# Kernel tuning notes

Measured on AMD Instinct MI355X. Metric: run time of the kernel, lower is better.

Reference implementation:

```python
import jax, jax.numpy as jnp
import numpy as np

D_LATENT = 2048
RANK = 16

def setup_inputs() -> dict:
    key = jax.random.key(0)
    k1, k2, k3 = jax.random.split(key, 3)
    h = jax.random.normal(k1, (4, 4096, D_LATENT), dtype=jnp.float32)
    # LoRA params: original init is randn/50 for A, zeros for B; use randn/50 for
    # both so the output is non-trivial for correctness testing.
    mat_A = jax.random.normal(k2, (D_LATENT, RANK), dtype=jnp.float32) / 50.0
    mat_B = jax.random.normal(k3, (RANK, D_LATENT), dtype=jnp.float32) / 50.0
    return {"h": h, "mat_A": mat_A, "mat_B": mat_B}

def reference(h, mat_A, mat_B):
    # Faithful to torch: F.linear(h, A @ B) == h @ (A @ B).T
    W = mat_A @ mat_B                      # [d_latent, d_latent]
    return jnp.einsum('bsd,ed->bse', h, W)  # h @ W.T
```

## Files before the change

kernel.cpp:

```cpp
#include <hip/hip_runtime.h>
#include <hip/hip_bf16.h>

typedef float f4 __attribute__((ext_vector_type(4)));
typedef short bf16x8 __attribute__((ext_vector_type(8)));

#define D 2048
#define RANK 16
#define NT 512

__device__ __forceinline__ short bf16_of(float x) {
    return __builtin_bit_cast(short, __float2bfloat16(x));
}

__device__ __forceinline__ bf16x8 cvt8(f4 lo, f4 hi) {
    bf16x8 r;
    r[0] = bf16_of(lo.x); r[1] = bf16_of(lo.y);
    r[2] = bf16_of(lo.z); r[3] = bf16_of(lo.w);
    r[4] = bf16_of(hi.x); r[5] = bf16_of(hi.y);
    r[6] = bf16_of(hi.z); r[7] = bf16_of(hi.w);
    return r;
}

__device__ __forceinline__ float bf2f(short s) {
    return __uint_as_float(((unsigned)(unsigned short)s) << 16);
}

__device__ __forceinline__ void barrier_lgkm() {
    asm volatile("s_waitcnt lgkmcnt(0)" ::: "memory");
    __builtin_amdgcn_s_barrier();
}

__global__ __launch_bounds__(NT, 4)
void lora_v7(const float* __restrict__ h, const float* __restrict__ A,
             const float* __restrict__ B, float* __restrict__ out) {
    const int tid  = threadIdx.x;
    const int wave = tid >> 6;
    const int lane = tid & 63;
    const int m16  = lane & 15;
    const int kg   = lane >> 4;
    const long row0 = (long)blockIdx.x * 16;

    __shared__ f4 ldsT[8][16][4];
    __shared__ f4 tt[16][4];

    bf16x8 Abf[4][2];
#pragma unroll
    for (int j = 0; j < 4; ++j) {
        const float* pa = A + (long)(tid * 4 + j) * RANK;
        f4 a0 = *(const f4*)(pa);
        f4 a1 = *(const f4*)(pa + 4);
        f4 a2 = *(const f4*)(pa + 8);
        f4 a3 = *(const f4*)(pa + 12);
        Abf[j][0] = cvt8(a0, a1);
        Abf[j][1] = cvt8(a2, a3);
    }

    const float* pB = B + (long)m16 * D + wave * 256 + kg * 8;
    bf16x8 Bb[8];
#pragma unroll
    for (int s = 0; s < 8; ++s) {
        f4 b0 = *(const f4*)(pB + s * 32);
        f4 b1 = *(const f4*)(pB + s * 32 + 4);
        Bb[s] = cvt8(b0, b1);
    }

    const float* ph = h + (row0 + m16) * D + wave * 256 + kg * 8;
    f4 hv[16];
#pragma unroll
    for (int s = 0; s < 8; ++s) {
        hv[2 * s]     = *(const f4*)(ph + s * 32);
        hv[2 * s + 1] = *(const f4*)(ph + s * 32 + 4);
    }
    f4 a0 = {0.f, 0.f, 0.f, 0.f}, a1 = {0.f, 0.f, 0.f, 0.f};
#pragma unroll
    for (int s = 0; s < 4; ++s)
        a0 = __builtin_amdgcn_mfma_f32_16x16x32_bf16(
            Bb[s], cvt8(hv[2 * s], hv[2 * s + 1]), a0, 0, 0, 0);
#pragma unroll
    for (int s = 4; s < 8; ++s)
        a1 = __builtin_amdgcn_mfma_f32_16x16x32_bf16(
            Bb[s], cvt8(hv[2 * s], hv[2 * s + 1]), a1, 0, 0, 0);
    ldsT[wave][m16][kg] = a0 + a1;

    barrier_lgkm();
    if (tid < 64) {
        const int r = tid >> 2, q = tid & 3;
        f4 s = ldsT[0][r][q];
#pragma unroll
        for (int w = 1; w < 8; ++w) s += ldsT[w][r][q];
        tt[r][q] = s;
    }
    barrier_lgkm();

    float* po = out + row0 * D + tid * 4;
#pragma unroll 4
    for (int r = 0; r < 16; ++r) {
        const f4 t0 = tt[r][0], t1 = tt[r][1];
        const f4 t2 = tt[r][2], t3 = tt[r][3];
        f4 res;
#pragma unroll
        for (int j = 0; j < 4; ++j) {
            const bf16x8 lo = Abf[j][0], hi = Abf[j][1];
            float v;
            v  = t0.x * bf2f(lo[0]) + t0.y * bf2f(lo[1]) +
                 t0.z * bf2f(lo[2]) + t0.w * bf2f(lo[3]);
            v += t1.x * bf2f(lo[4]) + t1.y * bf2f(lo[5]) +
                 t1.z * bf2f(lo[6]) + t1.w * bf2f(lo[7]);
            v += t2.x * bf2f(hi[0]) + t2.y * bf2f(hi[1]) +
                 t2.z * bf2f(hi[2]) + t2.w * bf2f(hi[3]);
            v += t3.x * bf2f(hi[4]) + t3.y * bf2f(hi[5]) +
                 t3.z * bf2f(hi[6]) + t3.w * bf2f(hi[7]);
            res[j] = v;
        }
        __builtin_nontemporal_store(res, (f4*)(po + (long)r * D));
    }
}

extern "C" void kernel_launch(void* const* d_in, const int* in_sizes, int n_in,
                              void* d_out, int out_size, void* d_ws,
                              size_t ws_size, hipStream_t stream) {
    const float* h = (const float*)d_in[0];
    const float* A = (const float*)d_in[1];
    const float* B = (const float*)d_in[2];
    float* out = (float*)d_out;

    const int n_rows = in_sizes[0] / D;
    const int blocks = n_rows / 16;

    hipLaunchKernelGGL(lora_v7, dim3(blocks), dim3(NT), 0, stream,
                       h, A, B, out);
}
```

Measured before the change: 64.20 us.

## Split fused LoRA kernel into separate down-projection and up-projection kernels

Replaces the single fused kernel with two launches. The first computes per-tile partial h·Bᵀ products with 256-thread blocks and writes them to workspace. The second reduces those partials and expands through A, with each thread covering two column groups. The aim is to separate the read-heavy phase from the write-heavy phase so each gets its own occupancy and traffic pattern. The cost is an extra launch plus a workspace round trip, and the fused kernel is kept as a fallback when the workspace is too small.

Result: slower. 180.4 us (+181.0%).

```diff
diff --git a/kernel.cpp b/kernel.cpp
--- a/kernel.cpp
+++ b/kernel.cpp
@@ -6,7 +6,8 @@
 
 #define D 2048
 #define RANK 16
-#define NT 512
+#define NT1 256
+#define NT2 256
 
 __device__ __forceinline__ short bf16_of(float x) {
     return __builtin_bit_cast(short, __float2bfloat16(x));
@@ -30,7 +31,110 @@
     __builtin_amdgcn_s_barrier();
 }
 
-__global__ __launch_bounds__(NT, 4)
+__global__ __launch_bounds__(NT1, 4)
+void lora_k1(const float* __restrict__ h, const float* __restrict__ B,
+             float* __restrict__ ws) {
+    const int tid  = threadIdx.x;
+    const int ks   = tid >> 6;
+    const int lane = tid & 63;
+    const int m16  = lane & 15;
+    const int kg   = lane >> 4;
+    const long tile = blockIdx.x;
+    const long row0 = tile * 16;
+
+    const float* pB = B + (long)m16 * D + ks * 512 + kg * 8;
+    const float* pH = h + (row0 + m16) * D + ks * 512 + kg * 8;
+
+    f4 a0 = {0.f, 0.f, 0.f, 0.f}, a1 = {0.f, 0.f, 0.f, 0.f};
+#pragma unroll
+    for (int s = 0; s < 8; ++s) {
+        f4 bl = *(const f4*)(pB + s * 32);
+        f4 bh = *(const f4*)(pB + s * 32 + 4);
+        f4 hl = *(const f4*)(pH + s * 32);
+        f4 hh = *(const f4*)(pH + s * 32 + 4);
+        a0 = __builtin_amdgcn_mfma_f32_16x16x32_bf16(
+            cvt8(bl, bh), cvt8(hl, hh), a0, 0, 0, 0);
+    }
+#pragma unroll
+    for (int s = 8; s < 16; ++s) {
+        f4 bl = *(const f4*)(pB + s * 32);
+        f4 bh = *(const f4*)(pB + s * 32 + 4);
+        f4 hl = *(const f4*)(pH + s * 32);
+        f4 hh = *(const f4*)(pH + s * 32 + 4);
+        a1 = __builtin_amdgcn_mfma_f32_16x16x32_bf16(
+            cvt8(bl, bh), cvt8(hl, hh), a1, 0, 0, 0);
+    }
+    const f4 acc = a0 + a1;
+    *(f4*)(ws + tile * 1024 + ks * 256 + m16 * 16 + kg * 4) = acc;
+}
+
+__global__ __launch_bounds__(NT2, 4)
+void lora_k2(const float* __restrict__ ws, const float* __restrict__ A,
+             float* __restrict__ out) {
+    const int tid  = threadIdx.x;
+    const int wave = tid >> 6;
+    const int lane = tid & 63;
+    const long tile = blockIdx.x;
+    const long row0 = tile * 16;
+
+    bf16x8 Abf[2][4][2];
+    int e0s[2];
+#pragma unroll
+    for (int si = 0; si < 2; ++si) {
+        const int e0 = (wave * 2 + si) * 256 + lane * 4;
+        e0s[si] = e0;
+#pragma unroll
+        for (int j = 0; j < 4; ++j) {
+            const float* pa = A + (long)(e0 + j) * RANK;
+            f4 q0 = *(const f4*)(pa);
+            f4 q1 = *(const f4*)(pa + 4);
+            f4 q2 = *(const f4*)(pa + 8);
+            f4 q3 = *(const f4*)(pa + 12);
+            Abf[si][j][0] = cvt8(q0, q1);
+            Abf[si][j][1] = cvt8(q2, q3);
+        }
+    }
+
+    __shared__ f4 pbuf[4][16][4];
+    __shared__ f4 tsum[16][4];
+    pbuf[tid >> 6][(tid >> 2) & 15][tid & 3] =
+        *(const f4*)(ws + tile * 1024 + tid * 4);
+    barrier_lgkm();
+    if (tid < 64) {
+        const int r = tid >> 2, q = tid & 3;
+        tsum[r][q] = pbuf[0][r][q] + pbuf[1][r][q] + pbuf[2][r][q] +
+                     pbuf[3][r][q];
+    }
+    barrier_lgkm();
+
+#pragma unroll 2
+    for (int r = 0; r < 16; ++r) {
+        const f4 t0 = tsum[r][0], t1 = tsum[r][1];
+        const f4 t2 = tsum[r][2], t3 = tsum[r][3];
+        float* po = out + (row0 + r) * D;
+#pragma unroll
+        for (int si = 0; si < 2; ++si) {
+            f4 res;
+#pragma unroll
+            for (int j = 0; j < 4; ++j) {
+                const bf16x8 lo = Abf[si][j][0], hi = Abf[si][j][1];
+                float v;
+                v  = t0.x * bf2f(lo[0]) + t0.y * bf2f(lo[1]) +
+                     t0.z * bf2f(lo[2]) + t0.w * bf2f(lo[3]);
+                v += t1.x * bf2f(lo[4]) + t1.y * bf2f(lo[5]) +
+                     t1.z * bf2f(lo[6]) + t1.w * bf2f(lo[7]);
+                v += t2.x * bf2f(hi[0]) + t2.y * bf2f(hi[1]) +
+                     t2.z * bf2f(hi[2]) + t2.w * bf2f(hi[3]);
+                v += t3.x * bf2f(hi[4]) + t3.y * bf2f(hi[5]) +
+                     t3.z * bf2f(hi[6]) + t3.w * bf2f(hi[7]);
+                res[j] = v;
+            }
+            __builtin_nontemporal_store(res, (f4*)(po + e0s[si]));
+        }
+    }
+}
+
+__global__ __launch_bounds__(512, 4)
 void lora_v7(const float* __restrict__ h, const float* __restrict__ A,
              const float* __restrict__ B, float* __restrict__ out) {
     const int tid  = threadIdx.x;
@@ -47,12 +151,12 @@
 #pragma unroll
     for (int j = 0; j < 4; ++j) {
         const float* pa = A + (long)(tid * 4 + j) * RANK;
-        f4 a0 = *(const f4*)(pa);
-        f4 a1 = *(const f4*)(pa + 4);
-        f4 a2 = *(const f4*)(pa + 8);
-        f4 a3 = *(const f4*)(pa + 12);
-        Abf[j][0] = cvt8(a0, a1);
-        Abf[j][1] = cvt8(a2, a3);
+        f4 q0 = *(const f4*)(pa);
+        f4 q1 = *(const f4*)(pa + 4);
+        f4 q2 = *(const f4*)(pa + 8);
+        f4 q3 = *(const f4*)(pa + 12);
+        Abf[j][0] = cvt8(q0, q1);
+        Abf[j][1] = cvt8(q2, q3);
     }
 
     const float* pB = B + (long)m16 * D + wave * 256 + kg * 8;
@@ -125,8 +229,17 @@
     float* out = (float*)d_out;
 
     const int n_rows = in_sizes[0] / D;
-    const int blocks = n_rows / 16;
-
-    hipLaunchKernelGGL(lora_v7, dim3(blocks), dim3(NT), 0, stream,
-                       h, A, B, out);
-}
+    const int tiles  = n_rows / 16;
+    const size_t ws_needed = (size_t)tiles * 1024 * sizeof(float);
+
+    if (ws_size >= ws_needed) {
+        float* ws = (float*)d_ws;
+        hipLaunchKernelGGL(lora_k1, dim3(tiles), dim3(NT1), 0, stream,
+                           h, B, ws);
+        hipLaunchKernelGGL(lora_k2, dim3(tiles), dim3(NT2), 0, stream,
+                           ws, A, out);
+    } else {
+        hipLaunchKernelGGL(lora_v7, dim3(tiles), dim3(512), 0, stream,
+                           h, A, B, out);
+    }
+}
```

## Stream h through double-buffered LDS via global_load_lds DMA over 4-row subtiles

Applied to the files above, without the earlier changes.

Each block now handles 32 rows instead of 16. It processes them as eight 4-row subtiles, loading h straight into an XOR-swizzled, double-buffered LDS buffer with global_load_lds so the next subtile's load overlaps the current subtile's MFMA and output stores. The goal is to hide global-load latency and keep reads and writes streaming at the same time. In exchange, each block uses 64KB of LDS, which lowers resident blocks per CU and halves the grid. It also adds two barriers per subtile, and the 16-row MFMA now works on 4 duplicated rows, wasting compute.

Result: slower. 85.15 us (+32.6%).

```diff
diff --git a/kernel.cpp b/kernel.cpp
--- a/kernel.cpp
+++ b/kernel.cpp
@@ -6,7 +6,9 @@
 
 #define D 2048
 #define RANK 16
-#define NT 512
+#define NTHR 512
+#define ROWS_PER_BLOCK 32
+#define NSUB 8
 
 __device__ __forceinline__ short bf16_of(float x) {
     return __builtin_bit_cast(short, __float2bfloat16(x));
@@ -30,90 +32,118 @@
     __builtin_amdgcn_s_barrier();
 }
 
-__global__ __launch_bounds__(NT, 4)
-void lora_v7(const float* __restrict__ h, const float* __restrict__ A,
-             const float* __restrict__ B, float* __restrict__ out) {
+__global__ __launch_bounds__(NTHR, 4)
+void lora_dma(const float* __restrict__ h, const float* __restrict__ A,
+              const float* __restrict__ B, float* __restrict__ out) {
+    __shared__ float hbuf[2][4 * D];
+    __shared__ f4 ldsT[8][16][4];
+    __shared__ f4 tt[4][4];
+
     const int tid  = threadIdx.x;
-    const int wave = tid >> 6;
+    const int w    = tid >> 6;
     const int lane = tid & 63;
     const int m16  = lane & 15;
     const int kg   = lane >> 4;
-    const long row0 = (long)blockIdx.x * 16;
-
-    __shared__ f4 ldsT[8][16][4];
-    __shared__ f4 tt[16][4];
+    const int row  = m16 & 3;
+    const long row0 = (long)blockIdx.x * ROWS_PER_BLOCK;
 
     bf16x8 Abf[4][2];
 #pragma unroll
     for (int j = 0; j < 4; ++j) {
         const float* pa = A + (long)(tid * 4 + j) * RANK;
-        f4 a0 = *(const f4*)(pa);
-        f4 a1 = *(const f4*)(pa + 4);
-        f4 a2 = *(const f4*)(pa + 8);
-        f4 a3 = *(const f4*)(pa + 12);
-        Abf[j][0] = cvt8(a0, a1);
-        Abf[j][1] = cvt8(a2, a3);
+        Abf[j][0] = cvt8(*(const f4*)(pa), *(const f4*)(pa + 4));
+        Abf[j][1] = cvt8(*(const f4*)(pa + 8), *(const f4*)(pa + 12));
     }
 
-    const float* pB = B + (long)m16 * D + wave * 256 + kg * 8;
+    const float* pB = B + (long)m16 * D + w * 256 + kg * 8;
     bf16x8 Bb[8];
 #pragma unroll
-    for (int s = 0; s < 8; ++s) {
-        f4 b0 = *(const f4*)(pB + s * 32);
-        f4 b1 = *(const f4*)(pB + s * 32 + 4);
-        Bb[s] = cvt8(b0, b1);
+    for (int s = 0; s < 8; ++s)
+        Bb[s] = cvt8(*(const f4*)(pB + s * 32), *(const f4*)(pB + s * 32 + 4));
+
+    const int rxor = (w >> 1) & 3;
+    const int glane = (lane ^ rxor) * 4;
+
+#define DMA_SUBTILE(bsel, st)                                                  \
+    {                                                                          \
+        const float* g_ = h + (row0 + (long)(st) * 4 + (w >> 1)) * D +         \
+                          (w & 1) * 1024 + glane;                              \
+        float* l_ = &hbuf[(bsel)][0] + w * 1024;                               \
+        _Pragma("unroll") for (int i = 0; i < 4; ++i)                          \
+            __builtin_amdgcn_global_load_lds(                                  \
+                (const __attribute__((address_space(1))) void*)(g_ + i * 256), \
+                (__attribute__((address_space(3))) void*)(l_ + i * 256),       \
+                16, 0, 0);                                                     \
     }
 
-    const float* ph = h + (row0 + m16) * D + wave * 256 + kg * 8;
-    f4 hv[16];
+    DMA_SUBTILE(0, 0)
+    asm volatile("s_waitcnt vmcnt(0)" ::: "memory");
+    __builtin_amdgcn_s_barrier();
+
+    const long rsh = row << 4;
+    const long rbase = (long)row * 8192;
+
+#pragma unroll 1
+    for (int t = 0; t < NSUB; ++t) {
+        if (t + 1 < NSUB) {
+            DMA_SUBTILE((t + 1) & 1, t + 1)
+            asm volatile("s_waitcnt vmcnt(8)" ::: "memory");
+        } else {
+            asm volatile("s_waitcnt vmcnt(4)" ::: "memory");
+        }
+        __builtin_amdgcn_s_barrier();
+
+        const char* hb = (const char*)&hbuf[t & 1][0];
+        f4 ac0 = {0.f, 0.f, 0.f, 0.f}, ac1 = {0.f, 0.f, 0.f, 0.f};
 #pragma unroll
-    for (int s = 0; s < 8; ++s) {
-        hv[2 * s]     = *(const f4*)(ph + s * 32);
-        hv[2 * s + 1] = *(const f4*)(ph + s * 32 + 4);
+        for (int s = 0; s < 8; ++s) {
+            const long c0 = (long)w * 1024 + kg * 32 + s * 128;
+            f4 v0 = *(const f4*)(hb + rbase + (c0 ^ rsh));
+            f4 v1 = *(const f4*)(hb + rbase + ((c0 + 16) ^ rsh));
+            bf16x8 hv = cvt8(v0, v1);
+            if (s < 4)
+                ac0 = __builtin_amdgcn_mfma_f32_16x16x32_bf16(Bb[s], hv, ac0,
+                                                              0, 0, 0);
+            else
+                ac1 = __builtin_amdgcn_mfma_f32_16x16x32_bf16(Bb[s], hv, ac1,
+                                                              0, 0, 0);
+        }
+        ldsT[w][m16][kg] = ac0 + ac1;
+
+        barrier_lgkm();
+        if (tid < 16) {
+            const int r = tid >> 2, q = tid & 3;
+            f4 s = ldsT[0][r][q];
+#pragma unroll
+            for (int ww = 1; ww < 8; ++ww) s += ldsT[ww][r][q];
+            tt[r][q] = s;
+        }
+        barrier_lgkm();
+
+        float* po = out + (row0 + (long)t * 4) * D + tid * 4;
+#pragma unroll
+        for (int r = 0; r < 4; ++r) {
+            const f4 t0 = tt[r][0], t1 = tt[r][1];
+            const f4 t2 = tt[r][2], t3 = tt[r][3];
+            f4 res;
+#pragma unroll
+            for (int j = 0; j < 4; ++j) {
+                const bf16x8 lo = Abf[j][0], hi = Abf[j][1];
+                float v;
+                v  = t0.x * bf2f(lo[0]) + t0.y * bf2f(lo[1]) +
+                     t0.z * bf2f(lo[2]) + t0.w * bf2f(lo[3]);
+                v += t1.x * bf2f(lo[4]) + t1.y * bf2f(lo[5]) +
+                     t1.z * bf2f(lo[6]) + t1.w * bf2f(lo[7]);
+                v += t2.x * bf2f(hi[0]) + t2.y * bf2f(hi[1]) +
+                     t2.z * bf2f(hi[2]) + t2.w * bf2f(hi[3]);
+                v += t3.x * bf2f(hi[4]) + t3.y * bf2f(hi[5]) +
+                     t3.z * bf2f(hi[6]) + t3.w * bf2f(hi[7]);
+                res[j] = v;
+            }
+            __builtin_nontemporal_store(res, (f4*)(po + (long)r * D));
+        }
     }
-    f4 a0 = {0.f, 0.f, 0.f, 0.f}, a1 = {0.f, 0.f, 0.f, 0.f};
-#pragma unroll
-    for (int s = 0; s < 4; ++s)
-        a0 = __builtin_amdgcn_mfma_f32_16x16x32_bf16(
-            Bb[s], cvt8(hv[2 * s], hv[2 * s + 1]), a0, 0, 0, 0);
-#pragma unroll
-    for (int s = 4; s < 8; ++s)
-        a1 = __builtin_amdgcn_mfma_f32_16x16x32_bf16(
-            Bb[s], cvt8(hv[2 * s], hv[2 * s + 1]), a1, 0, 0, 0);
-    ldsT[wave][m16][kg] = a0 + a1;
-
-    barrier_lgkm();
-    if (tid < 64) {
-        const int r = tid >> 2, q = tid & 3;
-        f4 s = ldsT[0][r][q];
-#pragma unroll
-        for (int w = 1; w < 8; ++w) s += ldsT[w][r][q];
-        tt[r][q] = s;
-    }
-    barrier_lgkm();
-
-    float* po = out + row0 * D + tid * 4;
-#pragma unroll 4
-    for (int r = 0; r < 16; ++r) {
-        const f4 t0 = tt[r][0], t1 = tt[r][1];
-        const f4 t2 = tt[r][2], t3 = tt[r][3];
-        f4 res;
-#pragma unroll
-        for (int j = 0; j < 4; ++j) {
-            const bf16x8 lo = Abf[j][0], hi = Abf[j][1];
-            float v;
-            v  = t0.x * bf2f(lo[0]) + t0.y * bf2f(lo[1]) +
-                 t0.z * bf2f(lo[2]) + t0.w * bf2f(lo[3]);
-            v += t1.x * bf2f(lo[4]) + t1.y * bf2f(lo[5]) +
-                 t1.z * bf2f(lo[6]) + t1.w * bf2f(lo[7]);
-            v += t2.x * bf2f(hi[0]) + t2.y * bf2f(hi[1]) +
-                 t2.z * bf2f(hi[2]) + t2.w * bf2f(hi[3]);
-            v += t3.x * bf2f(hi[4]) + t3.y * bf2f(hi[5]) +
-                 t3.z * bf2f(hi[6]) + t3.w * bf2f(hi[7]);
-            res[j] = v;
-        }
-        __builtin_nontemporal_store(res, (f4*)(po + (long)r * D));
-    }
+#undef DMA_SUBTILE
 }
 
 extern "C" void kernel_launch(void* const* d_in, const int* in_sizes, int n_in,
@@ -125,8 +155,8 @@
     float* out = (float*)d_out;
 
     const int n_rows = in_sizes[0] / D;
-    const int blocks = n_rows / 16;
+    const int blocks = n_rows / ROWS_PER_BLOCK;
 
-    hipLaunchKernelGGL(lora_v7, dim3(blocks), dim3(NT), 0, stream,
+    hipLaunchKernelGGL(lora_dma, dim3(blocks), dim3(NTHR), 0, stream,
                        h, A, B, out);
 }
```
